# Kernel optimization log

Hardware: AMD Instinct MI355X
Metric: run time of the kernel (lower is better)

Reference implementation:

```python
import jax, jax.numpy as jnp
import numpy as np

N_NODES = 100000
DEG = 16
N_EDGES = N_NODES * DEG
D_FEAT = 64
HIDDEN = 64
K_RATIO = 0.5  # self.k
EPS = 1e-08


@jax.custom_vjp
def binary_step(x):
    return (x > 0.0).astype(x.dtype)

def _bs_fwd(x):
    return binary_step(x), x

def _bs_bwd(x, g):
    ax = jnp.abs(x)
    # BinaryStep surrogate gradient: 0 for |x|>1, 0.4 for 0.4<|x|<=1, else 2-4|x|
    add = jnp.where(ax > 1.0, 0.0, jnp.where(ax > 0.4, 0.4, 2.0 - 4.0 * ax))
    return (g * add,)

binary_step.defvjp(_bs_fwd, _bs_bwd)


def segment_softmax(v, seg, n):
    # torch.sparse.softmax(dim=1) == softmax over edges grouped by row id
    m = jax.ops.segment_max(v, seg, num_segments=n)
    e = jnp.exp(v - m[seg])
    s = jax.ops.segment_sum(e, seg, num_segments=n)
    return e / s[seg]


def setup_inputs() -> dict:
    key = jax.random.key(0)
    k1, k2, k3, k4, k5, k6, k7 = jax.random.split(key, 7)
    # coalesced edge list: rows sorted, (row,col) unique, every node has DEG edges
    rows = np.repeat(np.arange(N_NODES, dtype=np.int32), DEG)
    offs = np.tile(np.arange(1, DEG + 1, dtype=np.int32), N_NODES)
    cols = ((rows + offs) % N_NODES).reshape(N_NODES, DEG)
    cols = np.sort(cols, axis=1).reshape(-1).astype(np.int32)
    indices = jnp.asarray(np.stack([rows, cols]))  # [2, E]
    features = jax.random.normal(k1, (N_NODES, D_FEAT), dtype=jnp.float32)
    values = jax.random.uniform(k2, (N_EDGES,), dtype=jnp.float32, minval=0.1, maxval=1.0)
    U = jax.random.uniform(k3, (N_EDGES,), dtype=jnp.float32)
    gumbel = -jnp.log(-jnp.log(U + EPS) + EPS)  # Gumbel(0,1) noise (precomputed for determinism)
    in_dim = 2 * D_FEAT + 1
    w0 = jax.random.normal(k4, (HIDDEN, in_dim), dtype=jnp.float32) * (6.0 / (in_dim + HIDDEN)) ** 0.5
    b0 = jax.random.normal(k5, (HIDDEN,), dtype=jnp.float32) * 0.02
    w1 = jax.random.normal(k6, (1, HIDDEN), dtype=jnp.float32) * (6.0 / (HIDDEN + 1)) ** 0.5
    b1 = jax.random.normal(k7, (1,), dtype=jnp.float32) * 0.02
    return {"features": features, "values": values, "w0": w0, "b0": b0,
            "w1": w1, "b1": b1, "gumbel": gumbel, "indices": indices,
            "n_nodes": N_NODES, "temperature": 1}


def reference(features, values, w0, b0, w1, b1, gumbel, indices, n_nodes, temperature):
    rows = indices[0]
    cols = indices[1]
    # gather endpoint features + edge weight, 2-layer MLP -> scalar score per edge
    temp = jnp.concatenate([features[rows], features[cols], values[:, None]], axis=-1)  # [E, 2D+1]
    h = jax.nn.relu(temp @ w0.T + b0)          # [E, H]
    z = (h @ w1.T + b1).reshape(-1)            # [E]
    z = z / jnp.maximum(jnp.linalg.norm(z), 1e-12)  # F.normalize(dim=0)
    pi = segment_softmax(z, rows, n_nodes)           # sparse row softmax
    logits = (jnp.log(pi) + gumbel) / temperature    # gumbel_softmax_sample (training path)
    y = segment_softmax(logits, rows, n_nodes)
    # per-node top-k threshold masking
    counts = jax.ops.segment_sum(jnp.ones_like(rows), rows, num_segments=n_nodes)  # [N]
    k_edges = jnp.maximum(jnp.round(counts.astype(y.dtype) * K_RATIO).astype(rows.dtype), 1)
    val_sort_idx = jnp.argsort(-y)                                   # global descending sort
    idx_sort_idx = jnp.argsort(rows[val_sort_idx], stable=True)      # stable regroup by row
    scores_sorted = y[val_sort_idx][idx_sort_idx]                    # per-row descending scores
    rows_sorted = rows[val_sort_idx][idx_sort_idx]
    edge_start = jnp.concatenate([jnp.zeros((1,), counts.dtype), jnp.cumsum(counts[:-1])])
    edge_end = jnp.abs(edge_start + k_edges - 1)
    node_thre = scores_sorted[edge_end]          # k-th largest score per node
    thre_aug = node_thre[rows_sorted]            # == repeat_interleave(counts) since rows_sorted ascending
    mask = binary_step(scores_sorted - thre_aug + 1e-12)
    masked = mask * scores_sorted
    masked = masked[jnp.argsort(idx_sort_idx)]   # undo row regroup
    masked = masked[jnp.argsort(val_sort_idx)]   # undo value sort -> original edge order
    return masked
```

## Files before the change

kernel.cpp:

```cpp
#include <hip/hip_runtime.h>

#define N_NODES 100000
#define DEG 16
#define N_EDGES (N_NODES * DEG)
#define NT 64
#define NBLK2 ((N_NODES + NT - 1) / NT)
#define NBLK_AB 1024
#define NPW 49

__global__ __launch_bounds__(256) void k_prep(const float* __restrict__ w0,
                                              float* __restrict__ w0T) {
    int id = blockIdx.x * 256 + threadIdx.x;
    if (id < 64 * 128) {
        int k = id >> 7, o = id & 127;
        w0T[k * 128 + o] = (o < 64) ? w0[o * 129 + k]
                                    : w0[(o - 64) * 129 + 64 + k];
    }
}

__global__ __launch_bounds__(256) void k_ab(const float* __restrict__ feat,
                                            const float* __restrict__ w0T,
                                            const float* __restrict__ b0,
                                            float* __restrict__ AB) {
    const int lane = threadIdx.x & 63;
    const int wid  = threadIdx.x >> 6;
    const int gw   = blockIdx.x * 4 + wid;
    const int half = gw & 1;
    const int wix  = gw >> 1;
    const int start = wix * NPW;
    if (start >= N_NODES) return;
    const int lim = min(start + NPW, N_NODES);

    float wreg[64];
#pragma unroll
    for (int k = 0; k < 64; ++k)
        wreg[k] = w0T[k * 128 + half * 64 + lane];

    const float b0v = (half == 0) ? b0[lane] : 0.f;

#define FMA8(ACC, X, Y, KC)                                   \
    ACC = fmaf(X.x, wreg[(KC) * 8 + 0], ACC);                 \
    ACC = fmaf(X.y, wreg[(KC) * 8 + 1], ACC);                 \
    ACC = fmaf(X.z, wreg[(KC) * 8 + 2], ACC);                 \
    ACC = fmaf(X.w, wreg[(KC) * 8 + 3], ACC);                 \
    ACC = fmaf(Y.x, wreg[(KC) * 8 + 4], ACC);                 \
    ACC = fmaf(Y.y, wreg[(KC) * 8 + 5], ACC);                 \
    ACC = fmaf(Y.z, wreg[(KC) * 8 + 6], ACC);                 \
    ACC = fmaf(Y.w, wreg[(KC) * 8 + 7], ACC);

#pragma unroll 1
    for (int nb = start; nb < lim; nb += 2) {
        const int n0u = __builtin_amdgcn_readfirstlane(nb);
        const int n1u = __builtin_amdgcn_readfirstlane((nb + 1 < lim) ? nb + 1 : nb);
        const float* f0 = feat + (size_t)n0u * 64;
        const float* f1 = feat + (size_t)n1u * 64;
        float a0 = 0.f, a1 = 0.f;
#pragma unroll
        for (int kc = 0; kc < 8; ++kc) {
            float4 x0 = *(const float4*)(f0 + kc * 8);
            float4 y0 = *(const float4*)(f0 + kc * 8 + 4);
            float4 x1 = *(const float4*)(f1 + kc * 8);
            float4 y1 = *(const float4*)(f1 + kc * 8 + 4);
            FMA8(a0, x0, y0, kc)
            FMA8(a1, x1, y1, kc)
        }
        AB[(size_t)n0u * 128 + half * 64 + lane] = a0 + b0v;
        AB[(size_t)n1u * 128 + half * 64 + lane] = a1 + b0v;
    }
#undef FMA8
}

__global__ __launch_bounds__(256) void k_edge(const float* __restrict__ AB,
                                              const float* __restrict__ values,
                                              const int* __restrict__ indices,
                                              const float* __restrict__ w0,
                                              const float* __restrict__ w1,
                                              const float* __restrict__ b1,
                                              float* __restrict__ z,
                                              double* __restrict__ partial) {
    __shared__ float b_s[80][68];
    __shared__ float wv_s[64];
    __shared__ float w1_s[64];
    __shared__ double redw[4];
    const int t = threadIdx.x;
    const int n0 = blockIdx.x * NT;
    const int nvalid = min(NT, N_NODES - n0);

    if (t < 64) {
        wv_s[t] = w0[t * 129 + 128];
        w1_s[t] = w1[t];
    }
    for (int idx = t; idx < 1280; idx += 256) {
        int r = idx >> 4, k4 = idx & 15;
        int node = n0 + 1 + r;
        if (node >= N_NODES) node -= N_NODES;
        *(float4*)&b_s[r][k4 * 4] = *(const float4*)(AB + (size_t)node * 128 + 64 + k4 * 4);
    }
    __syncthreads();

    const int row = t >> 2;
    const bool ok = row < nvalid;
    double ss = 0.0;
    if (ok) {
        const float* Ap = AB + (size_t)(n0 + row) * 128;
        const int ebase = n0 * 16 + (t << 2);
        int4   c4 = *(const int4*)(indices + N_EDGES + ebase);
        float4 v4 = *(const float4*)(values + ebase);
        int   cols[4] = {c4.x, c4.y, c4.z, c4.w};
        float vv[4]   = {v4.x, v4.y, v4.z, v4.w};
        int   ii[4];
        bool  fb[4];
        bool  anyfb = false;
#pragma unroll
        for (int k = 0; k < 4; ++k) {
            int i = cols[k] - (n0 + 1);
            if (i < 0) i += N_NODES;
            fb[k] = (i >= 80);
            anyfb |= fb[k];
            ii[k] = fb[k] ? 0 : i;
        }
        float acc[4] = {0.f, 0.f, 0.f, 0.f};
#pragma unroll
        for (int q = 0; q < 16; ++q) {
            float4 a4  = *(const float4*)(Ap + q * 4);
            float4 wv4 = *(const float4*)&wv_s[q * 4];
            float4 w14 = *(const float4*)&w1_s[q * 4];
#pragma unroll
            for (int k = 0; k < 4; ++k) {
                float4 b4 = *(const float4*)&b_s[ii[k]][q * 4];
                float t0 = fmaf(wv4.x, vv[k], a4.x + b4.x);
                float t1 = fmaf(wv4.y, vv[k], a4.y + b4.y);
                float t2 = fmaf(wv4.z, vv[k], a4.z + b4.z);
                float t3 = fmaf(wv4.w, vv[k], a4.w + b4.w);
                acc[k] = fmaf(w14.x, fmaxf(t0, 0.f), acc[k]);
                acc[k] = fmaf(w14.y, fmaxf(t1, 0.f), acc[k]);
                acc[k] = fmaf(w14.z, fmaxf(t2, 0.f), acc[k]);
                acc[k] = fmaf(w14.w, fmaxf(t3, 0.f), acc[k]);
            }
        }
        if (anyfb) {
#pragma unroll
            for (int k = 0; k < 4; ++k) {
                if (fb[k]) {
                    const float* Bp = AB + (size_t)cols[k] * 128 + 64;
                    float a = 0.f;
                    for (int h = 0; h < 64; ++h) {
                        float th = fmaf(wv_s[h], vv[k], Ap[h] + Bp[h]);
                        a = fmaf(w1_s[h], fmaxf(th, 0.f), a);
                    }
                    acc[k] = a;
                }
            }
        }
        const float b1v = b1[0];
        float4 z4;
        z4.x = acc[0] + b1v; z4.y = acc[1] + b1v;
        z4.z = acc[2] + b1v; z4.w = acc[3] + b1v;
        *(float4*)(z + ebase) = z4;
        ss = (double)z4.x * z4.x + (double)z4.y * z4.y +
             (double)z4.z * z4.z + (double)z4.w * z4.w;
    }
#pragma unroll
    for (int off = 32; off > 0; off >>= 1) ss += __shfl_down(ss, off, 64);
    if ((t & 63) == 0) redw[t >> 6] = ss;
    __syncthreads();
    if (t == 0) partial[blockIdx.x] = (redw[0] + redw[1]) + (redw[2] + redw[3]);
}

__global__ __launch_bounds__(256) void k_norm(const double* __restrict__ partial,
                                              double* __restrict__ nrm) {
    __shared__ double red[256];
    const int t = threadIdx.x;
    double s = 0.0;
    for (int i = t; i < NBLK2; i += 256) s += partial[i];
    red[t] = s;
    __syncthreads();
#pragma unroll
    for (int off = 128; off > 0; off >>= 1) {
        if (t < off) red[t] += red[t + off];
        __syncthreads();
    }
    if (t == 0) nrm[0] = fmax(sqrt(red[0]), 1e-12);
}

__global__ __launch_bounds__(256) void k_mask(const float* __restrict__ z,
                                              const float* __restrict__ gumbel,
                                              const double* __restrict__ nrm,
                                              const int* __restrict__ temperature,
                                              float* __restrict__ out) {
    const int n = blockIdx.x * 256 + threadIdx.x;
    if (n >= N_NODES) return;
    const double inv_nv = 1.0 / nrm[0];
    const double invT = 1.0 / (double)temperature[0];
    const float4* z4 = (const float4*)(z + (size_t)n * 16);
    const float4* g4 = (const float4*)(gumbel + (size_t)n * 16);
    double tl[16], y[16];
#pragma unroll
    for (int q = 0; q < 4; ++q) {
        float4 zv = z4[q];
        float4 gv = g4[q];
        tl[q * 4 + 0] = ((double)zv.x * inv_nv + (double)gv.x) * invT;
        tl[q * 4 + 1] = ((double)zv.y * inv_nv + (double)gv.y) * invT;
        tl[q * 4 + 2] = ((double)zv.z * inv_nv + (double)gv.z) * invT;
        tl[q * 4 + 3] = ((double)zv.w * inv_nv + (double)gv.w) * invT;
    }
    double m = tl[0];
#pragma unroll
    for (int i = 1; i < 16; ++i) m = fmax(m, tl[i]);
    double s = 0.0;
#pragma unroll
    for (int i = 0; i < 16; ++i) { y[i] = exp(tl[i] - m); s += y[i]; }
    const double inv_s = 1.0 / s;
#pragma unroll
    for (int i = 0; i < 16; ++i) y[i] *= inv_s;
    double thre = y[0];
#pragma unroll
    for (int i = 0; i < 16; ++i) {
        int c = 0, q = 0;
#pragma unroll
        for (int j = 0; j < 16; ++j) {
            c += (y[j] > y[i]) ? 1 : 0;
            q += (y[j] == y[i]) ? 1 : 0;
        }
        if (c <= 7 && 7 < c + q) thre = y[i];
    }
    float4* o4 = (float4*)(out + (size_t)n * 16);
#pragma unroll
    for (int qq = 0; qq < 4; ++qq) {
        float4 ov;
        ov.x = ((y[qq * 4 + 0] - thre + 1e-12) > 0.0) ? (float)y[qq * 4 + 0] : 0.f;
        ov.y = ((y[qq * 4 + 1] - thre + 1e-12) > 0.0) ? (float)y[qq * 4 + 1] : 0.f;
        ov.z = ((y[qq * 4 + 2] - thre + 1e-12) > 0.0) ? (float)y[qq * 4 + 2] : 0.f;
        ov.w = ((y[qq * 4 + 3] - thre + 1e-12) > 0.0) ? (float)y[qq * 4 + 3] : 0.f;
        o4[qq] = ov;
    }
}

extern "C" void kernel_launch(void* const* d_in, const int* in_sizes, int n_in,
                              void* d_out, int out_size, void* d_ws, size_t ws_size,
                              hipStream_t stream) {
    const float* feat    = (const float*)d_in[0];
    const float* values  = (const float*)d_in[1];
    const float* w0      = (const float*)d_in[2];
    const float* b0      = (const float*)d_in[3];
    const float* w1      = (const float*)d_in[4];
    const float* b1      = (const float*)d_in[5];
    const float* gumbel  = (const float*)d_in[6];
    const int*   indices = (const int*)d_in[7];
    const int*   temp    = (const int*)d_in[9];
    float* out = (float*)d_out;

    float*  w0T     = (float*)d_ws;
    float*  AB      = (float*)((char*)d_ws + 64 * 128 * 4);
    float*  zbuf    = (float*)((char*)d_ws + 64 * 128 * 4 + (size_t)N_NODES * 128 * 4);
    double* partial = (double*)((char*)d_ws + 64 * 128 * 4 + (size_t)N_NODES * 128 * 4
                                + (size_t)N_EDGES * 4);
    double* nrm     = partial + NBLK2;

    k_prep<<<32, 256, 0, stream>>>(w0, w0T);
    k_ab  <<<NBLK_AB, 256, 0, stream>>>(feat, w0T, b0, AB);
    k_edge<<<NBLK2, 256, 0, stream>>>(AB, values, indices, w0, w1, b1, zbuf, partial);
    k_norm<<<1, 256, 0, stream>>>(partial, nrm);
    k_mask<<<(N_NODES + 255) / 256, 256, 0, stream>>>(zbuf, gumbel, nrm, temp, out);
}
```

Baseline: 87.93 us.

## Halve edge-kernel shared tile, pin weight registers, double AB block count

The edge kernel now stages the neighbour B-half of AB through shared memory in two 32-column halves with extra barriers, cutting the LDS tile from 80x68 to 80x36 floats so more blocks can be resident per CU. The AB projection kernel replaces its weight array with 64 named scalars held in VGPRs by empty asm constraints, so the compiler cannot spill or re-index them. It also doubles its block count and halves nodes per wave for more parallelism. The cost is two extra __syncthreads per block and a serialized reload phase in the edge kernel.

```diff
diff --git a/kernel.cpp b/kernel.cpp
--- a/kernel.cpp
+++ b/kernel.cpp
@@ -5,8 +5,8 @@
 #define N_EDGES (N_NODES * DEG)
 #define NT 64
 #define NBLK2 ((N_NODES + NT - 1) / NT)
-#define NBLK_AB 1024
-#define NPW 49
+#define NBLK_AB 2048
+#define NPW 25
 
 __global__ __launch_bounds__(256) void k_prep(const float* __restrict__ w0,
                                               float* __restrict__ w0T) {
@@ -30,23 +30,42 @@
     const int start = wix * NPW;
     if (start >= N_NODES) return;
     const int lim = min(start + NPW, N_NODES);
-
-    float wreg[64];
-#pragma unroll
-    for (int k = 0; k < 64; ++k)
-        wreg[k] = w0T[k * 128 + half * 64 + lane];
+    const int c = half * 64 + lane;
+
+#define DECL8(p) float p##0, p##1, p##2, p##3, p##4, p##5, p##6, p##7;
+#define LOAD8(p, B)                                            \
+    p##0 = w0T[(B + 0) * 128 + c]; p##1 = w0T[(B + 1) * 128 + c]; \
+    p##2 = w0T[(B + 2) * 128 + c]; p##3 = w0T[(B + 3) * 128 + c]; \
+    p##4 = w0T[(B + 4) * 128 + c]; p##5 = w0T[(B + 5) * 128 + c]; \
+    p##6 = w0T[(B + 6) * 128 + c]; p##7 = w0T[(B + 7) * 128 + c];
+#define PIN8(p)                                                \
+    asm volatile("" : "+v"(p##0), "+v"(p##1), "+v"(p##2), "+v"(p##3), \
+                      "+v"(p##4), "+v"(p##5), "+v"(p##6), "+v"(p##7));
+
+    DECL8(wa) DECL8(wb) DECL8(wc) DECL8(wd)
+    DECL8(we) DECL8(wf) DECL8(wg) DECL8(wh)
+    LOAD8(wa, 0)  LOAD8(wb, 8)  LOAD8(wc, 16) LOAD8(wd, 24)
+    LOAD8(we, 32) LOAD8(wf, 40) LOAD8(wg, 48) LOAD8(wh, 56)
+    PIN8(wa) PIN8(wb) PIN8(wc) PIN8(wd)
+    PIN8(we) PIN8(wf) PIN8(wg) PIN8(wh)
 
     const float b0v = (half == 0) ? b0[lane] : 0.f;
 
-#define FMA8(ACC, X, Y, KC)                                   \
-    ACC = fmaf(X.x, wreg[(KC) * 8 + 0], ACC);                 \
-    ACC = fmaf(X.y, wreg[(KC) * 8 + 1], ACC);                 \
-    ACC = fmaf(X.z, wreg[(KC) * 8 + 2], ACC);                 \
-    ACC = fmaf(X.w, wreg[(KC) * 8 + 3], ACC);                 \
-    ACC = fmaf(Y.x, wreg[(KC) * 8 + 4], ACC);                 \
-    ACC = fmaf(Y.y, wreg[(KC) * 8 + 5], ACC);                 \
-    ACC = fmaf(Y.z, wreg[(KC) * 8 + 6], ACC);                 \
-    ACC = fmaf(Y.w, wreg[(KC) * 8 + 7], ACC);
+#define FMA8G(ACC, X, Y, p)                                   \
+    ACC = fmaf(X.x, p##0, ACC);  ACC = fmaf(X.y, p##1, ACC);  \
+    ACC = fmaf(X.z, p##2, ACC);  ACC = fmaf(X.w, p##3, ACC);  \
+    ACC = fmaf(Y.x, p##4, ACC);  ACC = fmaf(Y.y, p##5, ACC);  \
+    ACC = fmaf(Y.z, p##6, ACC);  ACC = fmaf(Y.w, p##7, ACC);
+
+#define CHUNK(p, KC)                                          \
+    {                                                         \
+        float4 x0 = *(const float4*)(f0 + (KC) * 8);          \
+        float4 y0 = *(const float4*)(f0 + (KC) * 8 + 4);      \
+        float4 x1 = *(const float4*)(f1 + (KC) * 8);          \
+        float4 y1 = *(const float4*)(f1 + (KC) * 8 + 4);      \
+        FMA8G(a0, x0, y0, p)                                  \
+        FMA8G(a1, x1, y1, p)                                  \
+    }
 
 #pragma unroll 1
     for (int nb = start; nb < lim; nb += 2) {
@@ -55,19 +74,11 @@
         const float* f0 = feat + (size_t)n0u * 64;
         const float* f1 = feat + (size_t)n1u * 64;
         float a0 = 0.f, a1 = 0.f;
-#pragma unroll
-        for (int kc = 0; kc < 8; ++kc) {
-            float4 x0 = *(const float4*)(f0 + kc * 8);
-            float4 y0 = *(const float4*)(f0 + kc * 8 + 4);
-            float4 x1 = *(const float4*)(f1 + kc * 8);
-            float4 y1 = *(const float4*)(f1 + kc * 8 + 4);
-            FMA8(a0, x0, y0, kc)
-            FMA8(a1, x1, y1, kc)
-        }
-        AB[(size_t)n0u * 128 + half * 64 + lane] = a0 + b0v;
-        AB[(size_t)n1u * 128 + half * 64 + lane] = a1 + b0v;
-    }
-#undef FMA8
+        CHUNK(wa, 0) CHUNK(wb, 1) CHUNK(wc, 2) CHUNK(wd, 3)
+        CHUNK(we, 4) CHUNK(wf, 5) CHUNK(wg, 6) CHUNK(wh, 7)
+        AB[(size_t)n0u * 128 + c] = a0 + b0v;
+        AB[(size_t)n1u * 128 + c] = a1 + b0v;
+    }
 }
 
 __global__ __launch_bounds__(256) void k_edge(const float* __restrict__ AB,
@@ -78,7 +89,7 @@
                                               const float* __restrict__ b1,
                                               float* __restrict__ z,
                                               double* __restrict__ partial) {
-    __shared__ float b_s[80][68];
+    __shared__ float b_s[80][36];
     __shared__ float wv_s[64];
     __shared__ float w1_s[64];
     __shared__ double redw[4];
@@ -90,27 +101,22 @@
         wv_s[t] = w0[t * 129 + 128];
         w1_s[t] = w1[t];
     }
-    for (int idx = t; idx < 1280; idx += 256) {
-        int r = idx >> 4, k4 = idx & 15;
-        int node = n0 + 1 + r;
-        if (node >= N_NODES) node -= N_NODES;
-        *(float4*)&b_s[r][k4 * 4] = *(const float4*)(AB + (size_t)node * 128 + 64 + k4 * 4);
-    }
-    __syncthreads();
 
     const int row = t >> 2;
     const bool ok = row < nvalid;
-    double ss = 0.0;
+    const int ebase = n0 * 16 + (t << 2);
+    int   cols[4] = {0, 0, 0, 0};
+    float vv[4]   = {0.f, 0.f, 0.f, 0.f};
+    int   ii[4]   = {0, 0, 0, 0};
+    bool  fb[4]   = {false, false, false, false};
+    bool  anyfb   = false;
+    float acc[4]  = {0.f, 0.f, 0.f, 0.f};
+    const float* Ap = AB + (size_t)(n0 + row) * 128;
     if (ok) {
-        const float* Ap = AB + (size_t)(n0 + row) * 128;
-        const int ebase = n0 * 16 + (t << 2);
         int4   c4 = *(const int4*)(indices + N_EDGES + ebase);
         float4 v4 = *(const float4*)(values + ebase);
-        int   cols[4] = {c4.x, c4.y, c4.z, c4.w};
-        float vv[4]   = {v4.x, v4.y, v4.z, v4.w};
-        int   ii[4];
-        bool  fb[4];
-        bool  anyfb = false;
+        cols[0] = c4.x; cols[1] = c4.y; cols[2] = c4.z; cols[3] = c4.w;
+        vv[0] = v4.x; vv[1] = v4.y; vv[2] = v4.z; vv[3] = v4.w;
 #pragma unroll
         for (int k = 0; k < 4; ++k) {
             int i = cols[k] - (n0 + 1);
@@ -119,25 +125,52 @@
             anyfb |= fb[k];
             ii[k] = fb[k] ? 0 : i;
         }
-        float acc[4] = {0.f, 0.f, 0.f, 0.f};
-#pragma unroll
-        for (int q = 0; q < 16; ++q) {
-            float4 a4  = *(const float4*)(Ap + q * 4);
-            float4 wv4 = *(const float4*)&wv_s[q * 4];
-            float4 w14 = *(const float4*)&w1_s[q * 4];
-#pragma unroll
-            for (int k = 0; k < 4; ++k) {
-                float4 b4 = *(const float4*)&b_s[ii[k]][q * 4];
-                float t0 = fmaf(wv4.x, vv[k], a4.x + b4.x);
-                float t1 = fmaf(wv4.y, vv[k], a4.y + b4.y);
-                float t2 = fmaf(wv4.z, vv[k], a4.z + b4.z);
-                float t3 = fmaf(wv4.w, vv[k], a4.w + b4.w);
-                acc[k] = fmaf(w14.x, fmaxf(t0, 0.f), acc[k]);
-                acc[k] = fmaf(w14.y, fmaxf(t1, 0.f), acc[k]);
-                acc[k] = fmaf(w14.z, fmaxf(t2, 0.f), acc[k]);
-                acc[k] = fmaf(w14.w, fmaxf(t3, 0.f), acc[k]);
-            }
-        }
+    }
+
+#define EDGE_Q(QG, BOFF)                                                   \
+    {                                                                      \
+        float4 a4  = *(const float4*)(Ap + (QG) * 4);                      \
+        float4 wv4 = *(const float4*)&wv_s[(QG) * 4];                      \
+        float4 w14 = *(const float4*)&w1_s[(QG) * 4];                      \
+        _Pragma("unroll")                                                  \
+        for (int k = 0; k < 4; ++k) {                                      \
+            float4 b4 = *(const float4*)&b_s[ii[k]][(BOFF) * 4];           \
+            float t0 = fmaf(wv4.x, vv[k], a4.x + b4.x);                    \
+            float t1 = fmaf(wv4.y, vv[k], a4.y + b4.y);                    \
+            float t2 = fmaf(wv4.z, vv[k], a4.z + b4.z);                    \
+            float t3 = fmaf(wv4.w, vv[k], a4.w + b4.w);                    \
+            acc[k] = fmaf(w14.x, fmaxf(t0, 0.f), acc[k]);                  \
+            acc[k] = fmaf(w14.y, fmaxf(t1, 0.f), acc[k]);                  \
+            acc[k] = fmaf(w14.z, fmaxf(t2, 0.f), acc[k]);                  \
+            acc[k] = fmaf(w14.w, fmaxf(t3, 0.f), acc[k]);                  \
+        }                                                                  \
+    }
+
+    for (int idx = t; idx < 640; idx += 256) {
+        int r = idx >> 3, k4 = idx & 7;
+        int node = n0 + 1 + r;
+        if (node >= N_NODES) node -= N_NODES;
+        *(float4*)&b_s[r][k4 * 4] =
+            *(const float4*)(AB + (size_t)node * 128 + 64 + k4 * 4);
+    }
+    __syncthreads();
+    if (ok) {
+        EDGE_Q(0, 0) EDGE_Q(1, 1) EDGE_Q(2, 2) EDGE_Q(3, 3)
+        EDGE_Q(4, 4) EDGE_Q(5, 5) EDGE_Q(6, 6) EDGE_Q(7, 7)
+    }
+    __syncthreads();
+    for (int idx = t; idx < 640; idx += 256) {
+        int r = idx >> 3, k4 = idx & 7;
+        int node = n0 + 1 + r;
+        if (node >= N_NODES) node -= N_NODES;
+        *(float4*)&b_s[r][k4 * 4] =
+            *(const float4*)(AB + (size_t)node * 128 + 96 + k4 * 4);
+    }
+    __syncthreads();
+    double ss = 0.0;
+    if (ok) {
+        EDGE_Q(8, 0)  EDGE_Q(9, 1)  EDGE_Q(10, 2) EDGE_Q(11, 3)
+        EDGE_Q(12, 4) EDGE_Q(13, 5) EDGE_Q(14, 6) EDGE_Q(15, 7)
         if (anyfb) {
 #pragma unroll
             for (int k = 0; k < 4; ++k) {
```

After: 89.83 us. 2.2% more time.
